# Kernel optimization log

Measured on AMD Instinct MI355X. Metric: run time of the kernel, lower is better.

The kernel has to match this reference:

```python
import jax, jax.numpy as jnp
import numpy as np

B, D, W = 2048, 512, 512
DEPTH = 6
N_BINS = 2 ** DEPTH          # 64 leaves
N_NODES = 2 ** DEPTH - 1     # 63 inner nodes


def build_indices(depth: int) -> np.ndarray:
    """Root-to-leaf path index table into hstack([probs, 1-probs]).
    Index j selects probs[:, j]; index j + N selects 1 - probs[:, j]."""
    n = 2 ** depth - 1
    paths = []
    for b in range(2 ** depth):
        node, path = 0, []
        for level in range(depth):
            bit = (b >> (depth - 1 - level)) & 1
            path.append(node if bit == 0 else node + n)
            node = 2 * node + 1 + bit
        paths.append(path)
    return np.asarray(paths, dtype=np.int32)  # [2**depth, depth]


def setup_inputs() -> dict:
    key = jax.random.key(0)
    k1, k2, k3, k4 = jax.random.split(key, 4)
    x = jax.random.normal(k1, (B, D), dtype=jnp.float32)
    ray = jax.random.normal(k2, (1, D), dtype=jnp.float32)  # kaiming-normal init
    w_i = jnp.zeros((1, N_NODES), dtype=jnp.float32)
    b_i = jax.random.normal(k3, (1, N_NODES), dtype=jnp.float32)
    a_i = 5.0 * jnp.ones((1, N_NODES), dtype=jnp.float32)
    # kaiming-normal over fan_in = input_width
    inner_transforms = jax.random.normal(k4, (N_BINS, D, W), dtype=jnp.float32) * np.float32((2.0 / D) ** 0.5)
    idx = jnp.asarray(build_indices(DEPTH))  # [64, 6] int32
    return {"x": x, "ray": ray, "w_i": w_i, "b_i": b_i, "a_i": a_i,
            "inner_transforms": inner_transforms, "idx": idx}


def reference(x, ray, w_i, b_i, a_i, inner_transforms, idx):
    eps = 1e-8
    # angles: arccos(cosine_similarity(x, ray)) / pi  -> [B]
    xn = jnp.maximum(jnp.linalg.norm(x, axis=1), eps)
    rn = jnp.maximum(jnp.linalg.norm(ray, axis=1), eps)  # [1]
    cos = (x @ ray[0]) / (xn * rn)
    angles = jnp.arccos(cos) / jnp.pi  # [B]
    # per-node decision probabilities: [B, N_NODES]
    node_fns = (0.5 + jax.nn.sigmoid(w_i)) * angles[:, None] - jax.nn.sigmoid(b_i)
    decisions = jax.nn.sigmoid(node_fns * (1.0 + a_i))
    # tree-indexed gather + product over path -> soft bin distribution [B, N_BINS]
    stacked = jnp.concatenate([decisions, 1.0 - decisions], axis=1)  # [B, 2N]
    bins, depth = idx.shape
    gathered = stacked[:, idx.reshape(-1)].reshape(x.shape[0], bins, depth)
    distribution = jnp.prod(gathered, axis=2)  # [B, L]
    # per-bin linear transforms, weighted by the distribution
    inner = jnp.einsum('bi,liw->blw', x, inner_transforms)  # [B, L, W]
    return jnp.einsum('bl,blo->bo', distribution, inner)  # [B, W]
```

## Files before the change

### kernel.cpp

```cpp
#include <hip/hip_runtime.h>
#include <math.h>

typedef float  f32x4  __attribute__((ext_vector_type(4)));
typedef short  bf16x8 __attribute__((ext_vector_type(8)));
typedef unsigned short u16x8 __attribute__((ext_vector_type(8)));
typedef unsigned short u16x4 __attribute__((ext_vector_type(4)));

#define B_ROWS 2048
#define D_DIM  512
#define W_DIM  512
#define N_NODES 63
#define N_BINS  64
#define K_TOT   32768
#define NSPLIT  16
#define LPS     (N_BINS / NSPLIT)
#define DEPS    1e-12f

__device__ __forceinline__ unsigned short f2bf(float f) {
    union { float f; unsigned int u; } v; v.f = f;
    unsigned int u = v.u;
    return (unsigned short)((u + 0x7fffu + ((u >> 16) & 1u)) >> 16);
}

__device__ __forceinline__ float sigmoidf_(float z) {
    return 1.0f / (1.0f + expf(-z));
}

__device__ __forceinline__ void load_lds16(const void* g, void* l) {
    __builtin_amdgcn_global_load_lds(
        (const __attribute__((address_space(1))) unsigned int*)g,
        (__attribute__((address_space(3))) unsigned int*)l,
        16, 0, 0);
}

__global__ __launch_bounds__(256) void k_pre(
    const float* __restrict__ x, const float* __restrict__ ray,
    const float* __restrict__ w_i, const float* __restrict__ b_i,
    const float* __restrict__ a_i, const int* __restrict__ idx,
    const float* __restrict__ T,
    float* __restrict__ dist, unsigned short* __restrict__ xb,
    unsigned short* __restrict__ Tt)
{
    __shared__ float tile[64][65];
    const int bid = blockIdx.x;
    const int t   = threadIdx.x;

    if (bid < 4096) {
        const int i0 = (bid & 7) * 64;
        const int w0 = ((bid >> 3) & 7) * 64;
        const int l  = bid >> 6;

        const int w4 = (t & 15) * 4;
        const int ir = t >> 4;
        const float* src = T + ((size_t)(l * 512 + i0)) * 512 + w0;
#pragma unroll
        for (int p = 0; p < 4; ++p) {
            int i = ir + p * 16;
            f32x4 v = *(const f32x4*)(src + (size_t)i * 512 + w4);
            tile[i][w4 + 0] = v.x; tile[i][w4 + 1] = v.y;
            tile[i][w4 + 2] = v.z; tile[i][w4 + 3] = v.w;
        }
        __syncthreads();
#pragma unroll
        for (int rep = 0; rep < 2; ++rep) {
            int id = t + rep * 256;
            int w  = id >> 3;
            int c  = id & 7;
            u16x8 o;
#pragma unroll
            for (int j = 0; j < 8; ++j) o[j] = f2bf(tile[c * 8 + j][w]);
            *(u16x8*)(Tt + (size_t)(w0 + w) * K_TOT + l * 512 + i0 + c * 8) = o;
        }
        return;
    }

    const int pb   = bid - 4096;
    const int wid  = t >> 6;
    const int lane = t & 63;
    const int row  = pb * 4 + wid;
    const float* xr = x + (size_t)row * D_DIM;

    float dotv = 0.f, xx = 0.f, rr = 0.f;
#pragma unroll
    for (int j = 0; j < 2; ++j) {
        f32x4 xv = *(const f32x4*)(xr  + j * 256 + lane * 4);
        f32x4 rv = *(const f32x4*)(ray + j * 256 + lane * 4);
        dotv += xv.x * rv.x + xv.y * rv.y + xv.z * rv.z + xv.w * rv.w;
        xx   += xv.x * xv.x + xv.y * xv.y + xv.z * xv.z + xv.w * xv.w;
        rr   += rv.x * rv.x + rv.y * rv.y + rv.z * rv.z + rv.w * rv.w;
        u16x4 o;
        o[0] = f2bf(xv.x); o[1] = f2bf(xv.y); o[2] = f2bf(xv.z); o[3] = f2bf(xv.w);
        *(u16x4*)(xb + (size_t)row * D_DIM + j * 256 + lane * 4) = o;
    }
#pragma unroll
    for (int off = 1; off < 64; off <<= 1) {
        dotv += __shfl_xor(dotv, off, 64);
        xx   += __shfl_xor(xx,   off, 64);
        rr   += __shfl_xor(rr,   off, 64);
    }
    float xn = fmaxf(sqrtf(xx), 1e-8f);
    float rn = fmaxf(sqrtf(rr), 1e-8f);
    float cosv = dotv / (xn * rn);
    cosv = fminf(1.f, fmaxf(-1.f, cosv));
    float angle = acosf(cosv) * 0.31830988618379067f;

    float dec = 0.f;
    if (lane < N_NODES) {
        float sw = sigmoidf_(w_i[lane]);
        float sb = sigmoidf_(b_i[lane]);
        float nf = (0.5f + sw) * angle - sb;
        dec = sigmoidf_(nf * (1.0f + a_i[lane]));
    }

    float p = 1.f;
#pragma unroll
    for (int v = 0; v < 6; ++v) {
        int j = idx[lane * 6 + v];
        int node = (j < N_NODES) ? j : j - N_NODES;
        float d = __shfl(dec, node, 64);
        p *= (j < N_NODES) ? d : (1.0f - d);
    }
    dist[(size_t)row * N_BINS + lane] = p;
}

__global__ __launch_bounds__(256, 4) void k_gemm6(
    const unsigned short* __restrict__ xb, const unsigned short* __restrict__ Tt,
    const float* __restrict__ dist, float* __restrict__ part)
{
    __shared__ unsigned short As[128 * 64];
    __shared__ unsigned short Bs[128 * 64];
    __shared__ float Ds[128 * LPS];

    const int b   = blockIdx.x;
    const int xcd = b & 7;
    const int j   = b >> 3;
    const int combo = xcd * 8 + (j >> 4);
    const int mblk  = j & 15;
    const int bm0 = mblk * 128;
    const int bn0 = (combo & 3) * 128;
    const int z   = combo >> 2;
    const int l0  = z * LPS;

    const int t    = threadIdx.x;
    const int lane = t & 63;
    const int wid  = t >> 6;
    const int wm = wid >> 1, wn = wid & 1;
    const int lq = lane >> 4, lr = lane & 15;

    const int srow = t >> 3;
    const int c    = t & 7;

    if (t < 128) {
        f32x4 dv = *(const f32x4*)(dist + (size_t)(bm0 + t) * N_BINS + l0);
        *(f32x4*)&Ds[t * LPS] = dv;
    }
    __syncthreads();

    f32x4 acc[4][4];
#pragma unroll
    for (int a = 0; a < 4; ++a)
#pragma unroll
        for (int bb = 0; bb < 4; ++bb)
            acc[a][bb] = (f32x4){0.f, 0.f, 0.f, 0.f};

    for (int lo = 0; lo < LPS; ++lo) {
        const int l = l0 + lo;

        if (lo > 0) {
#pragma unroll
            for (int fm = 0; fm < 4; ++fm)
#pragma unroll
                for (int r = 0; r < 4; ++r) {
                    int m = wm * 64 + fm * 16 + lq * 4 + r;
                    float dp = fmaxf(Ds[m * LPS + lo - 1], DEPS);
                    float dn = fmaxf(Ds[m * LPS + lo],     DEPS);
                    float ratio = dp * __builtin_amdgcn_rcpf(dn);
#pragma unroll
                    for (int fn = 0; fn < 4; ++fn)
                        acc[fm][fn][r] *= ratio;
                }
        }

        for (int it = 0; it < 8; ++it) {
            const int i0 = it * 64;
#pragma unroll
            for (int jj = 0; jj < 4; ++jj) {
                int row = srow + jj * 32;
                int cg  = c ^ (row & 7);
                load_lds16(xb + (size_t)(bm0 + row) * D_DIM + i0 + cg * 8,
                           &As[row * 64 + c * 8]);
                load_lds16(Tt + (size_t)(bn0 + row) * K_TOT + l * 512 + i0 + cg * 8,
                           &Bs[row * 64 + c * 8]);
            }
            __syncthreads();
#pragma unroll
            for (int ks = 0; ks < 2; ++ks) {
                bf16x8 af[4], bfr[4];
#pragma unroll
                for (int fm = 0; fm < 4; ++fm) {
                    int m = wm * 64 + fm * 16 + lr;
                    int g = ks * 4 + lq;
                    af[fm] = *(const bf16x8*)&As[m * 64 + ((g ^ (m & 7)) * 8)];
                }
#pragma unroll
                for (int fn = 0; fn < 4; ++fn) {
                    int n = wn * 64 + fn * 16 + lr;
                    int g = ks * 4 + lq;
                    bfr[fn] = *(const bf16x8*)&Bs[n * 64 + ((g ^ (n & 7)) * 8)];
                }
#pragma unroll
                for (int fm = 0; fm < 4; ++fm)
#pragma unroll
                    for (int fn = 0; fn < 4; ++fn)
                        acc[fm][fn] = __builtin_amdgcn_mfma_f32_16x16x32_bf16(
                            af[fm], bfr[fn], acc[fm][fn], 0, 0, 0);
            }
            __syncthreads();
        }
    }

    float* Cp = part + (size_t)z * (B_ROWS * W_DIM);
#pragma unroll
    for (int fm = 0; fm < 4; ++fm)
#pragma unroll
        for (int r = 0; r < 4; ++r) {
            int m = wm * 64 + fm * 16 + lq * 4 + r;
            float dl = fmaxf(Ds[m * LPS + LPS - 1], DEPS);
#pragma unroll
            for (int fn = 0; fn < 4; ++fn) {
                int col = bn0 + wn * 64 + fn * 16 + lr;
                Cp[(size_t)(bm0 + m) * W_DIM + col] = acc[fm][fn][r] * dl;
            }
        }
}

__global__ __launch_bounds__(256) void k_reduce(
    const float* __restrict__ part, float* __restrict__ out, int nsplit)
{
    int i = (blockIdx.x * 256 + threadIdx.x) * 4;
    f32x4 s = *(const f32x4*)(part + i);
    for (int p = 1; p < nsplit; ++p)
        s += *(const f32x4*)(part + (size_t)p * (B_ROWS * W_DIM) + i);
    *(f32x4*)(out + i) = s;
}

__global__ __launch_bounds__(256, 2) void k_gemm_bt(
    const float* __restrict__ x, const float* __restrict__ dist,
    const unsigned short* __restrict__ Tt, float* __restrict__ part,
    int kchunk)
{
    __shared__ unsigned short As[128][72];
    __shared__ unsigned short Bs[128][64];

    const int bm0 = blockIdx.x * 128;
    const int bn0 = blockIdx.y * 128;
    const int kbase = blockIdx.z * kchunk;

    const int lane = threadIdx.x & 63;
    const int wid  = threadIdx.x >> 6;
    const int wm = wid >> 1, wn = wid & 1;
    const int lq = lane >> 4, lr = lane & 15;

    f32x4 acc[4][4];
#pragma unroll
    for (int a = 0; a < 4; ++a)
#pragma unroll
        for (int b = 0; b < 4; ++b)
            acc[a][b] = (f32x4){0.f, 0.f, 0.f, 0.f};

    const int iters = kchunk / 64;
    for (int it = 0; it < iters; ++it) {
        const int k0 = kbase + it * 64;
        const int l  = k0 >> 9;
        const int i0 = k0 & 511;
#pragma unroll
        for (int r2 = 0; r2 < 8; ++r2) {
            int id = threadIdx.x + r2 * 256;
            int m  = id >> 4;
            int kc = id & 15;
            float sc = dist[(size_t)(bm0 + m) * N_BINS + l];
            f32x4 v = *(const f32x4*)(x + (size_t)(bm0 + m) * D_DIM + i0 + kc * 4);
            v *= sc;
            unsigned int p0 = (unsigned int)f2bf(v.x) | ((unsigned int)f2bf(v.y) << 16);
            unsigned int p1 = (unsigned int)f2bf(v.z) | ((unsigned int)f2bf(v.w) << 16);
            unsigned int* dp = (unsigned int*)&As[m][kc * 4];
            dp[0] = p0; dp[1] = p1;
        }
#pragma unroll
        for (int r2 = 0; r2 < 4; ++r2) {
            int id = threadIdx.x + r2 * 256;
            int n  = id >> 3;
            int cc = id & 7;
            int cg = cc ^ (n & 7);
            const u16x8 v = *(const u16x8*)(Tt + (size_t)(bn0 + n) * K_TOT + k0 + cg * 8);
            *(u16x8*)&Bs[n][cc * 8] = v;
        }
        __syncthreads();
#pragma unroll
        for (int ks = 0; ks < 2; ++ks) {
            bf16x8 af[4], bfr[4];
#pragma unroll
            for (int fm = 0; fm < 4; ++fm)
                af[fm] = *(const bf16x8*)&As[wm * 64 + fm * 16 + lr][ks * 32 + lq * 8];
#pragma unroll
            for (int fn = 0; fn < 4; ++fn) {
                int nl = wn * 64 + fn * 16 + lr;
                int cs = (ks * 4 + lq) ^ (nl & 7);
                bfr[fn] = *(const bf16x8*)&Bs[nl][cs * 8];
            }
#pragma unroll
            for (int fm = 0; fm < 4; ++fm)
#pragma unroll
                for (int fn = 0; fn < 4; ++fn)
                    acc[fm][fn] = __builtin_amdgcn_mfma_f32_16x16x32_bf16(
                        af[fm], bfr[fn], acc[fm][fn], 0, 0, 0);
        }
        __syncthreads();
    }

    float* Cp = part + (size_t)blockIdx.z * (B_ROWS * W_DIM);
#pragma unroll
    for (int fm = 0; fm < 4; ++fm)
#pragma unroll
        for (int fn = 0; fn < 4; ++fn)
#pragma unroll
            for (int r = 0; r < 4; ++r) {
                int row = bm0 + wm * 64 + fm * 16 + lq * 4 + r;
                int col = bn0 + wn * 64 + fn * 16 + lr;
                Cp[(size_t)row * W_DIM + col] = acc[fm][fn][r];
            }
}

extern "C" void kernel_launch(void* const* d_in, const int* in_sizes, int n_in,
                              void* d_out, int out_size, void* d_ws, size_t ws_size,
                              hipStream_t stream) {
    const float* x   = (const float*)d_in[0];
    const float* ray = (const float*)d_in[1];
    const float* w_i = (const float*)d_in[2];
    const float* b_i = (const float*)d_in[3];
    const float* a_i = (const float*)d_in[4];
    const float* T   = (const float*)d_in[5];
    const int*   idx = (const int*)d_in[6];
    float* out = (float*)d_out;

    char* ws = (char*)d_ws;
    const size_t distBytes = (size_t)B_ROWS * N_BINS * 4;
    const size_t xbBytes   = (size_t)B_ROWS * D_DIM * 2;
    const size_t ttBytes   = (size_t)W_DIM * K_TOT * 2;
    const size_t partBytes = (size_t)B_ROWS * W_DIM * 4;

    float*          dist = (float*)ws;
    unsigned short* xb   = (unsigned short*)(ws + distBytes);
    unsigned short* Tt   = (unsigned short*)(ws + distBytes + xbBytes);

    if (ws_size >= distBytes + xbBytes + ttBytes + (size_t)NSPLIT * partBytes) {
        float* part = (float*)(ws + distBytes + xbBytes + ttBytes);

        k_pre<<<4096 + 512, 256, 0, stream>>>(x, ray, w_i, b_i, a_i, idx, T,
                                              dist, xb, Tt);
        k_gemm6<<<1024, 256, 0, stream>>>(xb, Tt, dist, part);
        k_reduce<<<(B_ROWS * W_DIM) / (256 * 4), 256, 0, stream>>>(part, out, NSPLIT);
    } else if (ws_size >= distBytes + xbBytes + ttBytes) {
        k_pre<<<4096 + 512, 256, 0, stream>>>(x, ray, w_i, b_i, a_i, idx, T,
                                              dist, xb, Tt);
        k_gemm_bt<<<dim3(16, 4, 1), 256, 0, stream>>>(x, dist, Tt, out, K_TOT);
    }
}
```

Baseline: 220.6 us.

## Fuse preprocessing, split-K GEMM and reduction into one cooperative kernel

Replaces the three-kernel sequence (transpose/convert plus dist computation, split-K GEMM, partial-sum reduction) with a single cooperative kernel of 1024 blocks that uses grid-wide syncs between phases. The aim is to remove kernel launch gaps and tail effects between stages. In exchange, every block must wait at two grid barriers, and co-residency requires 4 blocks per CU under launch bounds, which may constrain registers. The old three-kernel path stays as a fallback if the cooperative launch fails. The else branch now runs the split-K path even when the partial-sum workspace is too small, which could write out of bounds.

```diff
diff --git a/kernel.cpp b/kernel.cpp
--- a/kernel.cpp
+++ b/kernel.cpp
@@ -1,5 +1,8 @@
 #include <hip/hip_runtime.h>
+#include <hip/hip_cooperative_groups.h>
 #include <math.h>
+
+namespace cg = cooperative_groups;
 
 typedef float  f32x4  __attribute__((ext_vector_type(4)));
 typedef short  bf16x8 __attribute__((ext_vector_type(8)));
@@ -31,6 +34,222 @@
         (const __attribute__((address_space(1))) unsigned int*)g,
         (__attribute__((address_space(3))) unsigned int*)l,
         16, 0, 0);
+}
+
+__global__ __launch_bounds__(256, 4) void k_fused(
+    const float* __restrict__ x, const float* __restrict__ ray,
+    const float* __restrict__ w_i, const float* __restrict__ b_i,
+    const float* __restrict__ a_i, const int* __restrict__ idx,
+    const float* __restrict__ T,
+    float* __restrict__ dist, unsigned short* __restrict__ xb,
+    unsigned short* __restrict__ Tt, float* __restrict__ part,
+    float* __restrict__ out)
+{
+    __shared__ __align__(16) char smem[34816];
+    unsigned short* As = (unsigned short*)smem;
+    unsigned short* Bs = (unsigned short*)(smem + 16384);
+    float*          Ds = (float*)(smem + 32768);
+    float (*tile)[65]  = (float (*)[65])smem;
+
+    const int bid = blockIdx.x;
+    const int t   = threadIdx.x;
+
+    {
+        const int w4 = (t & 15) * 4;
+        const int ir = t >> 4;
+        for (int q = 0; q < 4; ++q) {
+            const int job = bid * 4 + q;
+            const int i0 = (job & 7) * 64;
+            const int w0 = ((job >> 3) & 7) * 64;
+            const int l  = job >> 6;
+            const float* src = T + ((size_t)(l * 512 + i0)) * 512 + w0;
+#pragma unroll
+            for (int p = 0; p < 4; ++p) {
+                int i = ir + p * 16;
+                f32x4 v = *(const f32x4*)(src + (size_t)i * 512 + w4);
+                tile[i][w4 + 0] = v.x; tile[i][w4 + 1] = v.y;
+                tile[i][w4 + 2] = v.z; tile[i][w4 + 3] = v.w;
+            }
+            __syncthreads();
+#pragma unroll
+            for (int rep = 0; rep < 2; ++rep) {
+                int id = t + rep * 256;
+                int w  = id >> 3;
+                int c  = id & 7;
+                u16x8 o;
+#pragma unroll
+                for (int jj = 0; jj < 8; ++jj) o[jj] = f2bf(tile[c * 8 + jj][w]);
+                *(u16x8*)(Tt + (size_t)(w0 + w) * K_TOT + l * 512 + i0 + c * 8) = o;
+            }
+            __syncthreads();
+        }
+    }
+
+    if (bid < 512) {
+        const int wid  = t >> 6;
+        const int lane = t & 63;
+        const int row  = bid * 4 + wid;
+        const float* xr = x + (size_t)row * D_DIM;
+
+        float dotv = 0.f, xx = 0.f, rr = 0.f;
+#pragma unroll
+        for (int j = 0; j < 2; ++j) {
+            f32x4 xv = *(const f32x4*)(xr  + j * 256 + lane * 4);
+            f32x4 rv = *(const f32x4*)(ray + j * 256 + lane * 4);
+            dotv += xv.x * rv.x + xv.y * rv.y + xv.z * rv.z + xv.w * rv.w;
+            xx   += xv.x * xv.x + xv.y * xv.y + xv.z * xv.z + xv.w * xv.w;
+            rr   += rv.x * rv.x + rv.y * rv.y + rv.z * rv.z + rv.w * rv.w;
+            u16x4 o;
+            o[0] = f2bf(xv.x); o[1] = f2bf(xv.y); o[2] = f2bf(xv.z); o[3] = f2bf(xv.w);
+            *(u16x4*)(xb + (size_t)row * D_DIM + j * 256 + lane * 4) = o;
+        }
+#pragma unroll
+        for (int off = 1; off < 64; off <<= 1) {
+            dotv += __shfl_xor(dotv, off, 64);
+            xx   += __shfl_xor(xx,   off, 64);
+            rr   += __shfl_xor(rr,   off, 64);
+        }
+        float xn = fmaxf(sqrtf(xx), 1e-8f);
+        float rn = fmaxf(sqrtf(rr), 1e-8f);
+        float cosv = dotv / (xn * rn);
+        cosv = fminf(1.f, fmaxf(-1.f, cosv));
+        float angle = acosf(cosv) * 0.31830988618379067f;
+
+        float dec = 0.f;
+        if (lane < N_NODES) {
+            float sw = sigmoidf_(w_i[lane]);
+            float sb = sigmoidf_(b_i[lane]);
+            float nf = (0.5f + sw) * angle - sb;
+            dec = sigmoidf_(nf * (1.0f + a_i[lane]));
+        }
+
+        float p = 1.f;
+#pragma unroll
+        for (int v = 0; v < 6; ++v) {
+            int j = idx[lane * 6 + v];
+            int node = (j < N_NODES) ? j : j - N_NODES;
+            float d = __shfl(dec, node, 64);
+            p *= (j < N_NODES) ? d : (1.0f - d);
+        }
+        dist[(size_t)row * N_BINS + lane] = p;
+    }
+
+    __threadfence();
+    cg::this_grid().sync();
+
+    {
+        const int xcd = bid & 7;
+        const int j   = bid >> 3;
+        const int combo = xcd * 8 + (j >> 4);
+        const int mblk  = j & 15;
+        const int bm0 = mblk * 128;
+        const int bn0 = (combo & 3) * 128;
+        const int z   = combo >> 2;
+        const int l0  = z * LPS;
+
+        const int lane = t & 63;
+        const int wid  = t >> 6;
+        const int wm = wid >> 1, wn = wid & 1;
+        const int lq = lane >> 4, lr = lane & 15;
+
+        const int srow = t >> 3;
+        const int c    = t & 7;
+
+        if (t < 128) {
+            f32x4 dv = *(const f32x4*)(dist + (size_t)(bm0 + t) * N_BINS + l0);
+            *(f32x4*)&Ds[t * LPS] = dv;
+        }
+        __syncthreads();
+
+        f32x4 acc[4][4];
+#pragma unroll
+        for (int a = 0; a < 4; ++a)
+#pragma unroll
+            for (int bb = 0; bb < 4; ++bb)
+                acc[a][bb] = (f32x4){0.f, 0.f, 0.f, 0.f};
+
+        for (int lo = 0; lo < LPS; ++lo) {
+            const int l = l0 + lo;
+
+            if (lo > 0) {
+#pragma unroll
+                for (int fm = 0; fm < 4; ++fm)
+#pragma unroll
+                    for (int r = 0; r < 4; ++r) {
+                        int m = wm * 64 + fm * 16 + lq * 4 + r;
+                        float dp = fmaxf(Ds[m * LPS + lo - 1], DEPS);
+                        float dn = fmaxf(Ds[m * LPS + lo],     DEPS);
+                        float ratio = dp * __builtin_amdgcn_rcpf(dn);
+#pragma unroll
+                        for (int fn = 0; fn < 4; ++fn)
+                            acc[fm][fn][r] *= ratio;
+                    }
+            }
+
+            for (int it = 0; it < 8; ++it) {
+                const int i0 = it * 64;
+#pragma unroll
+                for (int jj = 0; jj < 4; ++jj) {
+                    int row = srow + jj * 32;
+                    int cg_ = c ^ (row & 7);
+                    load_lds16(xb + (size_t)(bm0 + row) * D_DIM + i0 + cg_ * 8,
+                               &As[row * 64 + c * 8]);
+                    load_lds16(Tt + (size_t)(bn0 + row) * K_TOT + l * 512 + i0 + cg_ * 8,
+                               &Bs[row * 64 + c * 8]);
+                }
+                __syncthreads();
+#pragma unroll
+                for (int ks = 0; ks < 2; ++ks) {
+                    bf16x8 af[4], bfr[4];
+#pragma unroll
+                    for (int fm = 0; fm < 4; ++fm) {
+                        int m = wm * 64 + fm * 16 + lr;
+                        int g = ks * 4 + lq;
+                        af[fm] = *(const bf16x8*)&As[m * 64 + ((g ^ (m & 7)) * 8)];
+                    }
+#pragma unroll
+                    for (int fn = 0; fn < 4; ++fn) {
+                        int n = wn * 64 + fn * 16 + lr;
+                        int g = ks * 4 + lq;
+                        bfr[fn] = *(const bf16x8*)&Bs[n * 64 + ((g ^ (n & 7)) * 8)];
+                    }
+#pragma unroll
+                    for (int fm = 0; fm < 4; ++fm)
+#pragma unroll
+                        for (int fn = 0; fn < 4; ++fn)
+                            acc[fm][fn] = __builtin_amdgcn_mfma_f32_16x16x32_bf16(
+                                af[fm], bfr[fn], acc[fm][fn], 0, 0, 0);
+                }
+                __syncthreads();
+            }
+        }
+
+        float* Cp = part + (size_t)z * (B_ROWS * W_DIM);
+#pragma unroll
+        for (int fm = 0; fm < 4; ++fm)
+#pragma unroll
+            for (int r = 0; r < 4; ++r) {
+                int m = wm * 64 + fm * 16 + lq * 4 + r;
+                float dl = fmaxf(Ds[m * LPS + LPS - 1], DEPS);
+#pragma unroll
+                for (int fn = 0; fn < 4; ++fn) {
+                    int col = bn0 + wn * 64 + fn * 16 + lr;
+                    Cp[(size_t)(bm0 + m) * W_DIM + col] = acc[fm][fn][r] * dl;
+                }
+            }
+    }
+
+    __threadfence();
+    cg::this_grid().sync();
+
+    {
+        int i = (bid * 256 + t) * 4;
+        f32x4 s = *(const f32x4*)(part + i);
+#pragma unroll
+        for (int p = 1; p < NSPLIT; ++p)
+            s += *(const f32x4*)(part + (size_t)p * (B_ROWS * W_DIM) + i);
+        *(f32x4*)(out + i) = s;
+    }
 }
 
 __global__ __launch_bounds__(256) void k_pre(
@@ -165,7 +384,6 @@
 
     for (int lo = 0; lo < LPS; ++lo) {
         const int l = l0 + lo;
-
         if (lo > 0) {
 #pragma unroll
             for (int fm = 0; fm < 4; ++fm)
@@ -186,10 +404,10 @@
 #pragma unroll
             for (int jj = 0; jj < 4; ++jj) {
                 int row = srow + jj * 32;
-                int cg  = c ^ (row & 7);
-                load_lds16(xb + (size_t)(bm0 + row) * D_DIM + i0 + cg * 8,
+                int cg_ = c ^ (row & 7);
+                load_lds16(xb + (size_t)(bm0 + row) * D_DIM + i0 + cg_ * 8,
                            &As[row * 64 + c * 8]);
-                load_lds16(Tt + (size_t)(bn0 + row) * K_TOT + l * 512 + i0 + cg * 8,
+                load_lds16(Tt + (size_t)(bn0 + row) * K_TOT + l * 512 + i0 + cg_ * 8,
                            &Bs[row * 64 + c * 8]);
             }
             __syncthreads();
@@ -242,93 +460,6 @@
     for (int p = 1; p < nsplit; ++p)
         s += *(const f32x4*)(part + (size_t)p * (B_ROWS * W_DIM) + i);
     *(f32x4*)(out + i) = s;
-}
-
-__global__ __launch_bounds__(256, 2) void k_gemm_bt(
-    const float* __restrict__ x, const float* __restrict__ dist,
-    const unsigned short* __restrict__ Tt, float* __restrict__ part,
-    int kchunk)
-{
-    __shared__ unsigned short As[128][72];
-    __shared__ unsigned short Bs[128][64];
-
-    const int bm0 = blockIdx.x * 128;
-    const int bn0 = blockIdx.y * 128;
-    const int kbase = blockIdx.z * kchunk;
-
-    const int lane = threadIdx.x & 63;
-    const int wid  = threadIdx.x >> 6;
-    const int wm = wid >> 1, wn = wid & 1;
-    const int lq = lane >> 4, lr = lane & 15;
-
-    f32x4 acc[4][4];
-#pragma unroll
-    for (int a = 0; a < 4; ++a)
-#pragma unroll
-        for (int b = 0; b < 4; ++b)
-            acc[a][b] = (f32x4){0.f, 0.f, 0.f, 0.f};
-
-    const int iters = kchunk / 64;
-    for (int it = 0; it < iters; ++it) {
-        const int k0 = kbase + it * 64;
-        const int l  = k0 >> 9;
-        const int i0 = k0 & 511;
-#pragma unroll
-        for (int r2 = 0; r2 < 8; ++r2) {
-            int id = threadIdx.x + r2 * 256;
-            int m  = id >> 4;
-            int kc = id & 15;
-            float sc = dist[(size_t)(bm0 + m) * N_BINS + l];
-            f32x4 v = *(const f32x4*)(x + (size_t)(bm0 + m) * D_DIM + i0 + kc * 4);
-            v *= sc;
-            unsigned int p0 = (unsigned int)f2bf(v.x) | ((unsigned int)f2bf(v.y) << 16);
-            unsigned int p1 = (unsigned int)f2bf(v.z) | ((unsigned int)f2bf(v.w) << 16);
-            unsigned int* dp = (unsigned int*)&As[m][kc * 4];
-            dp[0] = p0; dp[1] = p1;
-        }
-#pragma unroll
-        for (int r2 = 0; r2 < 4; ++r2) {
-            int id = threadIdx.x + r2 * 256;
-            int n  = id >> 3;
-            int cc = id & 7;
-            int cg = cc ^ (n & 7);
-            const u16x8 v = *(const u16x8*)(Tt + (size_t)(bn0 + n) * K_TOT + k0 + cg * 8);
-            *(u16x8*)&Bs[n][cc * 8] = v;
-        }
-        __syncthreads();
-#pragma unroll
-        for (int ks = 0; ks < 2; ++ks) {
-            bf16x8 af[4], bfr[4];
-#pragma unroll
-            for (int fm = 0; fm < 4; ++fm)
-                af[fm] = *(const bf16x8*)&As[wm * 64 + fm * 16 + lr][ks * 32 + lq * 8];
-#pragma unroll
-            for (int fn = 0; fn < 4; ++fn) {
-                int nl = wn * 64 + fn * 16 + lr;
-                int cs = (ks * 4 + lq) ^ (nl & 7);
-                bfr[fn] = *(const bf16x8*)&Bs[nl][cs * 8];
-            }
-#pragma unroll
-            for (int fm = 0; fm < 4; ++fm)
-#pragma unroll
-                for (int fn = 0; fn < 4; ++fn)
-                    acc[fm][fn] = __builtin_amdgcn_mfma_f32_16x16x32_bf16(
-                        af[fm], bfr[fn], acc[fm][fn], 0, 0, 0);
-        }
-        __syncthreads();
-    }
-
-    float* Cp = part + (size_t)blockIdx.z * (B_ROWS * W_DIM);
-#pragma unroll
-    for (int fm = 0; fm < 4; ++fm)
-#pragma unroll
-        for (int fn = 0; fn < 4; ++fn)
-#pragma unroll
-            for (int r = 0; r < 4; ++r) {
-                int row = bm0 + wm * 64 + fm * 16 + lq * 4 + r;
-                int col = bn0 + wn * 64 + fn * 16 + lr;
-                Cp[(size_t)row * W_DIM + col] = acc[fm][fn][r];
-            }
 }
 
 extern "C" void kernel_launch(void* const* d_in, const int* in_sizes, int n_in,
@@ -356,13 +487,25 @@
     if (ws_size >= distBytes + xbBytes + ttBytes + (size_t)NSPLIT * partBytes) {
         float* part = (float*)(ws + distBytes + xbBytes + ttBytes);
 
+        void* args[] = {
+            (void*)&x, (void*)&ray, (void*)&w_i, (void*)&b_i, (void*)&a_i,
+            (void*)&idx, (void*)&T, (void*)&dist, (void*)&xb, (void*)&Tt,
+            (void*)&part, (void*)&out
+        };
+        hipError_t e = hipLaunchCooperativeKernel(
+            (const void*)k_fused, dim3(1024), dim3(256), args, 0, stream);
+
+        if (e != hipSuccess) {
+            k_pre<<<4096 + 512, 256, 0, stream>>>(x, ray, w_i, b_i, a_i, idx, T,
+                                                  dist, xb, Tt);
+            k_gemm6<<<1024, 256, 0, stream>>>(xb, Tt, dist, part);
+            k_reduce<<<(B_ROWS * W_DIM) / (256 * 4), 256, 0, stream>>>(part, out, NSPLIT);
+        }
+    } else {
+        float* part = (float*)(ws + distBytes + xbBytes + ttBytes);
         k_pre<<<4096 + 512, 256, 0, stream>>>(x, ray, w_i, b_i, a_i, idx, T,
                                               dist, xb, Tt);
         k_gemm6<<<1024, 256, 0, stream>>>(xb, Tt, dist, part);
         k_reduce<<<(B_ROWS * W_DIM) / (256 * 4), 256, 0, stream>>>(part, out, NSPLIT);
-    } else if (ws_size >= distBytes + xbBytes + ttBytes) {
-        k_pre<<<4096 + 512, 256, 0, stream>>>(x, ray, w_i, b_i, a_i, idx, T,
-                                              dist, xb, Tt);
-        k_gemm_bt<<<dim3(16, 4, 1), 256, 0, stream>>>(x, dist, Tt, out, K_TOT);
-    }
-}
+    }
+}
```

Result: slower. 657.2 us (+197.9%).

## Double-buffer LDS tiles in split-K GEMM and read dist from global

Applied to the files above, without the earlier changes.

Flattens the per-bin and per-K-chunk loops into one loop and double-buffers the A/B shared-memory tiles. The next tile's global-to-LDS load is issued before the MFMAs on the current tile, and one barrier per iteration replaces two. The shared-memory copy of the distribution values is dropped, and the rescaling ratios are read directly from global memory. Shared memory use doubles and the launch bound drops from 4 to 2 blocks per CU, so there is less occupancy to hide latency.

```diff
diff --git a/kernel.cpp b/kernel.cpp
--- a/kernel.cpp
+++ b/kernel.cpp
@@ -2,6 +2,7 @@
 #include <math.h>
 
 typedef float  f32x4  __attribute__((ext_vector_type(4)));
+typedef float  f32x2  __attribute__((ext_vector_type(2)));
 typedef short  bf16x8 __attribute__((ext_vector_type(8)));
 typedef unsigned short u16x8 __attribute__((ext_vector_type(8)));
 typedef unsigned short u16x4 __attribute__((ext_vector_type(4)));
@@ -123,13 +124,12 @@
     dist[(size_t)row * N_BINS + lane] = p;
 }
 
-__global__ __launch_bounds__(256, 4) void k_gemm6(
+__global__ __launch_bounds__(256, 2) void k_gemm8(
     const unsigned short* __restrict__ xb, const unsigned short* __restrict__ Tt,
     const float* __restrict__ dist, float* __restrict__ part)
 {
-    __shared__ unsigned short As[128 * 64];
-    __shared__ unsigned short Bs[128 * 64];
-    __shared__ float Ds[128 * LPS];
+    __shared__ unsigned short As[2][128 * 64];
+    __shared__ unsigned short Bs[2][128 * 64];
 
     const int b   = blockIdx.x;
     const int xcd = b & 7;
@@ -150,12 +150,6 @@
     const int srow = t >> 3;
     const int c    = t & 7;
 
-    if (t < 128) {
-        f32x4 dv = *(const f32x4*)(dist + (size_t)(bm0 + t) * N_BINS + l0);
-        *(f32x4*)&Ds[t * LPS] = dv;
-    }
-    __syncthreads();
-
     f32x4 acc[4][4];
 #pragma unroll
     for (int a = 0; a < 4; ++a)
@@ -163,17 +157,40 @@
         for (int bb = 0; bb < 4; ++bb)
             acc[a][bb] = (f32x4){0.f, 0.f, 0.f, 0.f};
 
-    for (int lo = 0; lo < LPS; ++lo) {
-        const int l = l0 + lo;
-
-        if (lo > 0) {
+    const int NIT = LPS * 8;
+
+#define STAGE(it_, buf_)                                                      \
+    {                                                                         \
+        const int l_  = l0 + ((it_) >> 3);                                    \
+        const int i0_ = ((it_) & 7) * 64;                                     \
+        _Pragma("unroll")                                                     \
+        for (int jj = 0; jj < 4; ++jj) {                                      \
+            int row = srow + jj * 32;                                         \
+            int cg_ = c ^ (row & 7);                                          \
+            load_lds16(xb + (size_t)(bm0 + row) * D_DIM + i0_ + cg_ * 8,      \
+                       &As[buf_][row * 64 + c * 8]);                          \
+            load_lds16(Tt + (size_t)(bn0 + row) * K_TOT + (size_t)l_ * 512    \
+                           + i0_ + cg_ * 8,                                   \
+                       &Bs[buf_][row * 64 + c * 8]);                          \
+        }                                                                     \
+    }
+
+    STAGE(0, 0);
+
+    for (int it = 0; it < NIT; ++it) {
+        __syncthreads();
+        if (it + 1 < NIT) STAGE(it + 1, (it + 1) & 1);
+
+        if ((it & 7) == 0 && it > 0) {
+            const int l = l0 + (it >> 3);
 #pragma unroll
             for (int fm = 0; fm < 4; ++fm)
 #pragma unroll
                 for (int r = 0; r < 4; ++r) {
-                    int m = wm * 64 + fm * 16 + lq * 4 + r;
-                    float dp = fmaxf(Ds[m * LPS + lo - 1], DEPS);
-                    float dn = fmaxf(Ds[m * LPS + lo],     DEPS);
+                    int m = bm0 + wm * 64 + fm * 16 + lq * 4 + r;
+                    f32x2 dd = *(const f32x2*)(dist + (size_t)m * N_BINS + (l - 1));
+                    float dp = fmaxf(dd.x, DEPS);
+                    float dn = fmaxf(dd.y, DEPS);
                     float ratio = dp * __builtin_amdgcn_rcpf(dn);
 #pragma unroll
                     for (int fn = 0; fn < 4; ++fn)
@@ -181,41 +198,28 @@
                 }
         }
 
-        for (int it = 0; it < 8; ++it) {
-            const int i0 = it * 64;
-#pragma unroll
-            for (int jj = 0; jj < 4; ++jj) {
-                int row = srow + jj * 32;
-                int cg  = c ^ (row & 7);
-                load_lds16(xb + (size_t)(bm0 + row) * D_DIM + i0 + cg * 8,
-                           &As[row * 64 + c * 8]);
-                load_lds16(Tt + (size_t)(bn0 + row) * K_TOT + l * 512 + i0 + cg * 8,
-                           &Bs[row * 64 + c * 8]);
-            }
-            __syncthreads();
-#pragma unroll
-            for (int ks = 0; ks < 2; ++ks) {
-                bf16x8 af[4], bfr[4];
-#pragma unroll
-                for (int fm = 0; fm < 4; ++fm) {
-                    int m = wm * 64 + fm * 16 + lr;
-                    int g = ks * 4 + lq;
-                    af[fm] = *(const bf16x8*)&As[m * 64 + ((g ^ (m & 7)) * 8)];
-                }
-#pragma unroll
-                for (int fn = 0; fn < 4; ++fn) {
-                    int n = wn * 64 + fn * 16 + lr;
-                    int g = ks * 4 + lq;
-                    bfr[fn] = *(const bf16x8*)&Bs[n * 64 + ((g ^ (n & 7)) * 8)];
-                }
-#pragma unroll
-                for (int fm = 0; fm < 4; ++fm)
-#pragma unroll
-                    for (int fn = 0; fn < 4; ++fn)
-                        acc[fm][fn] = __builtin_amdgcn_mfma_f32_16x16x32_bf16(
-                            af[fm], bfr[fn], acc[fm][fn], 0, 0, 0);
-            }
-            __syncthreads();
+        const int buf = it & 1;
+#pragma unroll
+        for (int ks = 0; ks < 2; ++ks) {
+            bf16x8 af[4], bfr[4];
+#pragma unroll
+            for (int fm = 0; fm < 4; ++fm) {
+                int m = wm * 64 + fm * 16 + lr;
+                int g = ks * 4 + lq;
+                af[fm] = *(const bf16x8*)&As[buf][m * 64 + ((g ^ (m & 7)) * 8)];
+            }
+#pragma unroll
+            for (int fn = 0; fn < 4; ++fn) {
+                int n = wn * 64 + fn * 16 + lr;
+                int g = ks * 4 + lq;
+                bfr[fn] = *(const bf16x8*)&Bs[buf][n * 64 + ((g ^ (n & 7)) * 8)];
+            }
+#pragma unroll
+            for (int fm = 0; fm < 4; ++fm)
+#pragma unroll
+                for (int fn = 0; fn < 4; ++fn)
+                    acc[fm][fn] = __builtin_amdgcn_mfma_f32_16x16x32_bf16(
+                        af[fm], bfr[fn], acc[fm][fn], 0, 0, 0);
         }
     }
 
@@ -224,14 +228,15 @@
     for (int fm = 0; fm < 4; ++fm)
 #pragma unroll
         for (int r = 0; r < 4; ++r) {
-            int m = wm * 64 + fm * 16 + lq * 4 + r;
-            float dl = fmaxf(Ds[m * LPS + LPS - 1], DEPS);
+            int m = bm0 + wm * 64 + fm * 16 + lq * 4 + r;
+            float dl = fmaxf(dist[(size_t)m * N_BINS + (l0 + LPS - 1)], DEPS);
 #pragma unroll
             for (int fn = 0; fn < 4; ++fn) {
                 int col = bn0 + wn * 64 + fn * 16 + lr;
-                Cp[(size_t)(bm0 + m) * W_DIM + col] = acc[fm][fn][r] * dl;
-            }
-        }
+                Cp[(size_t)m * W_DIM + col] = acc[fm][fn][r] * dl;
+            }
+        }
+#undef STAGE
 }
 
 __global__ __launch_bounds__(256) void k_reduce(
@@ -358,7 +363,7 @@
 
         k_pre<<<4096 + 512, 256, 0, stream>>>(x, ray, w_i, b_i, a_i, idx, T,
                                               dist, xb, Tt);
-        k_gemm6<<<1024, 256, 0, stream>>>(xb, Tt, dist, part);
+        k_gemm8<<<1024, 256, 0, stream>>>(xb, Tt, dist, part);
         k_reduce<<<(B_ROWS * W_DIM) / (256 * 4), 256, 0, stream>>>(part, out, NSPLIT);
     } else if (ws_size >= distBytes + xbBytes + ttBytes) {
         k_pre<<<4096 + 512, 256, 0, stream>>>(x, ray, w_i, b_i, a_i, idx, T,
```

Result: faster. 200.4 us (-9.2%).
